# Performance work log

Hardware: AMD Instinct MI355X
Metric: run time of the kernel (lower is better)

## Reference

```python
import jax, jax.numpy as jnp
import numpy as np

B, S, D, H = 16, 577, 768, 12  # batch, seq (24*24+1 cls), hidden, heads
WH, WW = 24, 24
HEAD = D // H
NUM_REL = (2 * WH - 1) * (2 * WW - 1) + 3  # 2212


def make_rel_pos_index(wh, ww):
    # mirrors TFData2VecVisionRelativePositionBias.get_position_index
    xx, yy = np.meshgrid(np.arange(wh), np.arange(ww))  # 'xy' indexing like tf.meshgrid
    coords = np.stack([yy, xx], axis=0).reshape(2, -1)  # [2, wh*ww]
    rel = coords[:, :, None] - coords[:, None, :]       # [2, N, N]
    rel = rel.transpose(1, 2, 0)                        # [N, N, 2]
    rx = (rel[:, :, 0] + wh - 1) * (2 * ww - 1)
    ry = rel[:, :, 1] + ww - 1
    idx = rx + ry                                       # [N, N]
    n = idx.shape[0]
    top = np.full((1, n), NUM_REL - 3, dtype=idx.dtype)
    left = np.full((n, 1), NUM_REL - 2, dtype=idx.dtype)
    corner = np.full((1, 1), NUM_REL - 1, dtype=idx.dtype)
    idx = np.concatenate([top, idx], axis=0)
    idx = np.concatenate([np.concatenate([corner, left], axis=0), idx], axis=1)
    return idx.astype(np.int32)  # [N+1, N+1]


def setup_inputs() -> dict:
    key = jax.random.key(0)
    ks = jax.random.split(key, 6)
    scale = 0.02
    return {
        "hidden_states": jax.random.normal(ks[0], (B, S, D), jnp.float32),
        "Wq": jax.random.normal(ks[1], (D, D), jnp.float32) * scale,
        "bq": jnp.zeros((D,), jnp.float32),
        "Wk": jax.random.normal(ks[2], (D, D), jnp.float32) * scale,
        "Wv": jax.random.normal(ks[3], (D, D), jnp.float32) * scale,
        "bv": jnp.zeros((D,), jnp.float32),
        "rel_pos_bias_table": jax.random.normal(ks[4], (NUM_REL, H), jnp.float32) * scale,
        "rel_pos_index": jnp.asarray(make_rel_pos_index(WH, WW)),
    }


def reference(hidden_states, Wq, bq, Wk, Wv, bv, rel_pos_bias_table, rel_pos_index):
    b, s, _ = hidden_states.shape
    q = (hidden_states @ Wq + bq).reshape(b, s, H, HEAD).transpose(0, 2, 1, 3)
    k = (hidden_states @ Wk).reshape(b, s, H, HEAD).transpose(0, 2, 1, 3)
    v = (hidden_states @ Wv + bv).reshape(b, s, H, HEAD).transpose(0, 2, 1, 3)
    scores = jnp.einsum("bhqd,bhkd->bhqk", q, k) / jnp.sqrt(jnp.float32(HEAD))
    # gathered relative position bias: [S, S, H] -> [H, S, S]
    bias = rel_pos_bias_table[rel_pos_index].transpose(2, 0, 1)
    scores = scores + bias[None]
    probs = jax.nn.softmax(scores, axis=-1)
    out = jnp.einsum("bhqk,bhkd->bhqd", probs, v)
    out = out.transpose(0, 2, 1, 3).reshape(b, s, D)
    return out
```

## Files before the change

kernel.cpp:

```cpp
#include <hip/hip_runtime.h>
#include <hip/hip_bf16.h>


typedef __attribute__((ext_vector_type(8))) short bf16x8;
typedef __attribute__((ext_vector_type(4))) float f32x4;
typedef unsigned short u16;

#define SEQ 577
#define MTOT 9232
#define QKV_STRIDE 7090176
#define VT_PITCH 640
#define B_PITCH 640

static __device__ __forceinline__ u16 f2bf(float x) {
  unsigned int u = __float_as_uint(x);
  u = (u + 0x7FFFu + ((u >> 16) & 1u)) >> 16;
  return (u16)u;
}
static __device__ __forceinline__ float bf2f(u16 v) {
  return __uint_as_float(((unsigned int)v) << 16);
}

static __device__ __forceinline__ void gload_lds16(const void* g, void* l) {
  __builtin_amdgcn_global_load_lds(
      (const __attribute__((address_space(1))) unsigned int*)g,
      (__attribute__((address_space(3))) unsigned int*)l, 16, 0, 0);
}

__global__ __launch_bounds__(256) void transpose_w(
    const float* __restrict__ Wq, const float* __restrict__ Wk,
    const float* __restrict__ Wv, u16* __restrict__ WT) {
  __shared__ float t[32][33];
  const float* W = (blockIdx.z == 0) ? Wq : (blockIdx.z == 1) ? Wk : Wv;
  int x = threadIdx.x & 31;
  int y = threadIdx.x >> 5;
  int k0 = blockIdx.x * 32;
  int n0 = blockIdx.y * 32;
#pragma unroll
  for (int i = 0; i < 4; ++i)
    t[y + i * 8][x] = W[(size_t)(k0 + y + i * 8) * 768 + n0 + x];
  __syncthreads();
  u16* o = WT + (size_t)blockIdx.z * 589824;
#pragma unroll
  for (int i = 0; i < 4; ++i)
    o[(size_t)(n0 + y + i * 8) * 768 + k0 + x] = f2bf(t[x][y + i * 8]);
}

__global__ __launch_bounds__(256) void cvt_x(const float* __restrict__ X,
                                             u16* __restrict__ Xb) {
  size_t i = ((size_t)blockIdx.x * 256 + threadIdx.x) * 8;
  if (i >= (size_t)MTOT * 768) return;
  const float4* xp = (const float4*)(X + i);
  float4 a = xp[0], b = xp[1];
  u16 pk[8] = {f2bf(a.x), f2bf(a.y), f2bf(a.z), f2bf(a.w),
               f2bf(b.x), f2bf(b.y), f2bf(b.z), f2bf(b.w)};
  *(int4*)(Xb + i) = *(const int4*)pk;
}

__global__ __launch_bounds__(256) void bias_pre(
    const float* __restrict__ table, const int* __restrict__ idx,
    u16* __restrict__ biasm) {
  int q = blockIdx.x;
  int h = blockIdx.y;
  for (int k = threadIdx.x; k < B_PITCH; k += 256) {
    u16 v = 0;
    if (k < SEQ) v = f2bf(table[idx[q * SEQ + k] * 12 + h]);
    biasm[((size_t)h * SEQ + q) * B_PITCH + k] = v;
  }
}

__global__ __launch_bounds__(256) void transpose_v(
    const u16* __restrict__ v,
    u16* __restrict__ vT) {
  const int tile = blockIdx.x;
  const int bh = blockIdx.y;
  const int b = bh / 12, h = bh % 12;
  const int tid = threadIdx.x;
  __shared__ u16 T[128][64];
  const int s0 = tile * 128;
  const u16* vp = v + (size_t)b * SEQ * 768 + h * 64;
#pragma unroll
  for (int it = 0; it < 4; ++it) {
    int c = tid + it * 256;
    int r = c >> 3, ko = (c & 7) << 3;
    int gs = s0 + r;
    int4 val = make_int4(0, 0, 0, 0);
    if (gs < SEQ) val = *(const int4*)(vp + (size_t)gs * 768 + ko);
    *(int4*)&T[r][ko ^ (((r >> 3) & 7) << 3)] = val;
  }
  __syncthreads();
  u16* op = vT + (size_t)bh * 64 * VT_PITCH;
#pragma unroll
  for (int it = 0; it < 4; ++it) {
    int c = tid + it * 256;
    int d = c >> 4, so = (c & 15) << 3;
    u16 tmp[8];
#pragma unroll
    for (int j = 0; j < 8; ++j) {
      int rr = so + j;
      tmp[j] = T[rr][d ^ (((rr >> 3) & 7) << 3)];
    }
    *(int4*)(op + (size_t)d * VT_PITCH + s0 + so) = *(const int4*)tmp;
  }
}

__global__ __launch_bounds__(256) void qkv_gemm(
    const u16* __restrict__ Xb,
    const u16* __restrict__ WT,
    const float* __restrict__ bq, const float* __restrict__ bv,
    u16* __restrict__ qkv) {
  const int widx = blockIdx.z;
  const int m0 = blockIdx.x * 128;
  const int n0 = blockIdx.y * 128;
  const int tid = threadIdx.x;
  const int lane = tid & 63;
  const int w = tid >> 6;
  const int wm = (w >> 1) * 64;
  const int wn = (w & 1) * 64;
  const int quad = lane >> 4;
  const int l15 = lane & 15;

  __shared__ u16 As[128][32];
  __shared__ u16 Bs[128][32];

  const u16* Wp = WT + (size_t)widx * 589824;

  const int srow = w * 32 + (lane >> 2);
  const int scol = (lane & 3) * 8;

  f32x4 acc[4][4];
#pragma unroll
  for (int i = 0; i < 4; ++i)
#pragma unroll
    for (int j = 0; j < 4; ++j) acc[i][j] = (f32x4){0.f, 0.f, 0.f, 0.f};

  for (int kt = 0; kt < 24; ++kt) {
    const int k0 = kt * 32;
    {
      int r0 = m0 + srow;
      int r1 = r0 + 16;
      if (r0 > MTOT - 1) r0 = MTOT - 1;
      if (r1 > MTOT - 1) r1 = MTOT - 1;
      gload_lds16(Xb + (size_t)r0 * 768 + k0 + scol, &As[w * 32][0]);
      gload_lds16(Xb + (size_t)r1 * 768 + k0 + scol, &As[w * 32 + 16][0]);
      gload_lds16(Wp + (size_t)(n0 + srow) * 768 + k0 + scol, &Bs[w * 32][0]);
      gload_lds16(Wp + (size_t)(n0 + srow + 16) * 768 + k0 + scol, &Bs[w * 32 + 16][0]);
    }
    __syncthreads();
    bf16x8 af[4], bfv[4];
#pragma unroll
    for (int i = 0; i < 4; ++i)
      af[i] = *(const bf16x8*)(&As[wm + i * 16 + l15][quad * 8]);
#pragma unroll
    for (int i = 0; i < 4; ++i)
      bfv[i] = *(const bf16x8*)(&Bs[wn + i * 16 + l15][quad * 8]);
#pragma unroll
    for (int mt = 0; mt < 4; ++mt)
#pragma unroll
      for (int nt = 0; nt < 4; ++nt)
        acc[mt][nt] = __builtin_amdgcn_mfma_f32_16x16x32_bf16(af[mt], bfv[nt],
                                                              acc[mt][nt], 0, 0, 0);
    __syncthreads();
  }

  const float scale = (widx == 0) ? 0.125f : 1.0f;
  u16* ob = qkv + (size_t)widx * QKV_STRIDE;
#pragma unroll
  for (int nt = 0; nt < 4; ++nt) {
    int n = n0 + wn + nt * 16 + l15;
    float biasv = 0.f;
    if (widx == 0) biasv = bq[n] * 0.125f;
    else if (widx == 2) biasv = bv[n];
#pragma unroll
    for (int mt = 0; mt < 4; ++mt) {
#pragma unroll
      for (int r = 0; r < 4; ++r) {
        int m = m0 + wm + mt * 16 + quad * 4 + r;
        if (m < MTOT)
          ob[(size_t)m * 768 + n] = f2bf(acc[mt][nt][r] * scale + biasv);
      }
    }
  }
}

__global__ __launch_bounds__(256) void attn(
    const u16* __restrict__ qkv, const u16* __restrict__ vT,
    const u16* __restrict__ biasm, float* __restrict__ out) {
  const int bh = blockIdx.x;
  const int qt = blockIdx.y;
  const int b = bh / 12, h = bh - b * 12;
  const int tid = threadIdx.x;
  const int lane = tid & 63;
  const int w = tid >> 6;
  const int quad = lane >> 4;
  const int l15 = lane & 15;

  const u16* qp = qkv + (size_t)b * SEQ * 768 + h * 64;
  const u16* kp = qp + (size_t)QKV_STRIDE;
  const u16* vtp = vT + (size_t)bh * 64 * VT_PITCH;
  const u16* bp = biasm + (size_t)h * SEQ * B_PITCH;

  __shared__ u16 Ks[64][72];
  __shared__ u16 VTs[64][72];
  __shared__ u16 Ps[4][16][72];

  const int qrow0 = qt * 64 + w * 16;

  bf16x8 qf[2];
  {
    int row = qrow0 + l15;
    if (row > 576) row = 576;
    qf[0] = *(const bf16x8*)(qp + (size_t)row * 768 + quad * 8);
    qf[1] = *(const bf16x8*)(qp + (size_t)row * 768 + 32 + quad * 8);
  }
  int brow[4];
#pragma unroll
  for (int r = 0; r < 4; ++r) {
    int rr = qrow0 + quad * 4 + r;
    if (rr > 576) rr = 576;
    brow[r] = rr;
  }

  float lacc[4] = {0.f, 0.f, 0.f, 0.f};
  f32x4 O[4];
#pragma unroll
  for (int dt = 0; dt < 4; ++dt) O[dt] = (f32x4){0.f, 0.f, 0.f, 0.f};

  for (int kt = 0; kt < 10; ++kt) {
    const int kbase = kt * 64;
    u16 bb[4][4];
#pragma unroll
    for (int nt = 0; nt < 4; ++nt)
#pragma unroll
      for (int r = 0; r < 4; ++r)
        bb[nt][r] = bp[(size_t)brow[r] * B_PITCH + kbase + nt * 16 + l15];

#pragma unroll
    for (int it = 0; it < 2; ++it) {
      int c = tid + it * 256;
      int rr = c >> 3, ko = (c & 7) << 3;
      int gk = kbase + rr;
      int4 kvv = make_int4(0, 0, 0, 0);
      if (gk < SEQ) kvv = *(const int4*)(kp + (size_t)gk * 768 + ko);
      *(int4*)&Ks[rr][ko] = kvv;
      *(int4*)&VTs[rr][ko] = *(const int4*)(vtp + (size_t)rr * VT_PITCH + kbase + ko);
    }
    __syncthreads();

    f32x4 s[4];
#pragma unroll
    for (int nt = 0; nt < 4; ++nt) {
      f32x4 z = (f32x4){bf2f(bb[nt][0]), bf2f(bb[nt][1]),
                        bf2f(bb[nt][2]), bf2f(bb[nt][3])};
      bf16x8 kf0 = *(const bf16x8*)(&Ks[nt * 16 + l15][quad * 8]);
      bf16x8 kf1 = *(const bf16x8*)(&Ks[nt * 16 + l15][32 + quad * 8]);
      z = __builtin_amdgcn_mfma_f32_16x16x32_bf16(qf[0], kf0, z, 0, 0, 0);
      z = __builtin_amdgcn_mfma_f32_16x16x32_bf16(qf[1], kf1, z, 0, 0, 0);
      s[nt] = z;
    }

    const bool full = (kbase + 64 <= SEQ);
#pragma unroll
    for (int nt = 0; nt < 4; ++nt) {
#pragma unroll
      for (int r = 0; r < 4; ++r) {
        float p = __expf(s[nt][r]);
        unsigned int u = __float_as_uint(p);
        float pt = __uint_as_float(u & 0xFFFF0000u);
        if (full) lacc[r] += pt;
        else lacc[r] += ((kbase + nt * 16 + l15) < SEQ) ? pt : 0.f;
        Ps[w][quad * 4 + r][((nt ^ quad) << 4) + l15] = (u16)(u >> 16);
      }
    }

#pragma unroll
    for (int ks = 0; ks < 2; ++ks) {
      int cc = (ks * 32 + quad * 8) ^ ((l15 >> 2) << 4);
      bf16x8 pf = *(const bf16x8*)(&Ps[w][l15][cc]);
#pragma unroll
      for (int dt = 0; dt < 4; ++dt) {
        bf16x8 vf = *(const bf16x8*)(&VTs[dt * 16 + l15][ks * 32 + quad * 8]);
        O[dt] = __builtin_amdgcn_mfma_f32_16x16x32_bf16(pf, vf, O[dt], 0, 0, 0);
      }
    }
    __syncthreads();
  }

#pragma unroll
  for (int r = 0; r < 4; ++r) {
    float l = lacc[r];
    l += __shfl_xor(l, 1);
    l += __shfl_xor(l, 2);
    l += __shfl_xor(l, 4);
    l += __shfl_xor(l, 8);
    int row = qrow0 + quad * 4 + r;
    if (row < SEQ) {
      float inv = 1.f / l;
#pragma unroll
      for (int dt = 0; dt < 4; ++dt)
        out[((size_t)(b * SEQ + row)) * 768 + h * 64 + dt * 16 + l15] = O[dt][r] * inv;
    }
  }
}

extern "C" void kernel_launch(void* const* d_in, const int* in_sizes, int n_in,
                              void* d_out, int out_size, void* d_ws, size_t ws_size,
                              hipStream_t stream) {
  const float* hs = (const float*)d_in[0];
  const float* Wq = (const float*)d_in[1];
  const float* bq = (const float*)d_in[2];
  const float* Wk = (const float*)d_in[3];
  const float* Wv = (const float*)d_in[4];
  const float* bv = (const float*)d_in[5];
  const float* table = (const float*)d_in[6];
  const int* idx = (const int*)d_in[7];
  float* out = (float*)d_out;

  char* ws = (char*)d_ws;
  u16* qkv = (u16*)ws;
  u16* WT = (u16*)(ws + 42541056);
  u16* Xb = (u16*)(ws + 46080000);
  u16* vT = (u16*)(ws + 42541056);
  u16* biasm = (u16*)(ws + 58269696);

  hipLaunchKernelGGL(transpose_w, dim3(24, 24, 3), dim3(256), 0, stream, Wq, Wk, Wv, WT);
  hipLaunchKernelGGL(cvt_x, dim3(3462), dim3(256), 0, stream, hs, Xb);
  hipLaunchKernelGGL(qkv_gemm, dim3(73, 6, 3), dim3(256), 0, stream, Xb, WT, bq, bv, qkv);
  hipLaunchKernelGGL(bias_pre, dim3(577, 12), dim3(256), 0, stream, table, idx, biasm);
  hipLaunchKernelGGL(transpose_v, dim3(5, 192), dim3(256), 0, stream,
                     qkv + 2 * (size_t)QKV_STRIDE, vT);
  hipLaunchKernelGGL(attn, dim3(192, 10), dim3(256), 0, stream, qkv, vT, biasm, out);
}
```

Measured before the change: 237.2 us.

## Remap QKV GEMM blocks per XCD and stage epilogue through LDS for vector stores

The QKV GEMM launch becomes a 1D grid whose block index is remapped so that all 18 N/weight tiles of a given M row-tile run on the same XCD. This is meant to improve L2 reuse of the X tile. The epilogue now writes the bf16 results into a swizzled LDS buffer, reused from the operand tiles, in two halves, then emits 16-byte coalesced global stores instead of scattered 2-byte stores. The cost is extra barriers, some idle padded blocks (1440 launched versus 1314 needed), and only half the waves active during each LDS write phase.

```diff
diff --git a/kernel.cpp b/kernel.cpp
--- a/kernel.cpp
+++ b/kernel.cpp
@@ -109,9 +109,16 @@
     const u16* __restrict__ WT,
     const float* __restrict__ bq, const float* __restrict__ bv,
     u16* __restrict__ qkv) {
-  const int widx = blockIdx.z;
-  const int m0 = blockIdx.x * 128;
-  const int n0 = blockIdx.y * 128;
+  const int bid = blockIdx.x;
+  const int xcd = bid & 7;
+  const int local = bid >> 3;
+  const int mp = (local / 18) * 8 + xcd;
+  if (mp >= 73) return;
+  const int nw = local % 18;
+  const int widx = nw % 3;
+  const int m0 = mp * 128;
+  const int n0 = (nw / 3) * 128;
+
   const int tid = threadIdx.x;
   const int lane = tid & 63;
   const int w = tid >> 6;
@@ -120,8 +127,7 @@
   const int quad = lane >> 4;
   const int l15 = lane & 15;
 
-  __shared__ u16 As[128][32];
-  __shared__ u16 Bs[128][32];
+  __shared__ u16 SH[2][128][32];
 
   const u16* Wp = WT + (size_t)widx * 589824;
 
@@ -141,19 +147,19 @@
       int r1 = r0 + 16;
       if (r0 > MTOT - 1) r0 = MTOT - 1;
       if (r1 > MTOT - 1) r1 = MTOT - 1;
-      gload_lds16(Xb + (size_t)r0 * 768 + k0 + scol, &As[w * 32][0]);
-      gload_lds16(Xb + (size_t)r1 * 768 + k0 + scol, &As[w * 32 + 16][0]);
-      gload_lds16(Wp + (size_t)(n0 + srow) * 768 + k0 + scol, &Bs[w * 32][0]);
-      gload_lds16(Wp + (size_t)(n0 + srow + 16) * 768 + k0 + scol, &Bs[w * 32 + 16][0]);
+      gload_lds16(Xb + (size_t)r0 * 768 + k0 + scol, &SH[0][w * 32][0]);
+      gload_lds16(Xb + (size_t)r1 * 768 + k0 + scol, &SH[0][w * 32 + 16][0]);
+      gload_lds16(Wp + (size_t)(n0 + srow) * 768 + k0 + scol, &SH[1][w * 32][0]);
+      gload_lds16(Wp + (size_t)(n0 + srow + 16) * 768 + k0 + scol, &SH[1][w * 32 + 16][0]);
     }
     __syncthreads();
     bf16x8 af[4], bfv[4];
 #pragma unroll
     for (int i = 0; i < 4; ++i)
-      af[i] = *(const bf16x8*)(&As[wm + i * 16 + l15][quad * 8]);
+      af[i] = *(const bf16x8*)(&SH[0][wm + i * 16 + l15][quad * 8]);
 #pragma unroll
     for (int i = 0; i < 4; ++i)
-      bfv[i] = *(const bf16x8*)(&Bs[wn + i * 16 + l15][quad * 8]);
+      bfv[i] = *(const bf16x8*)(&SH[1][wn + i * 16 + l15][quad * 8]);
 #pragma unroll
     for (int mt = 0; mt < 4; ++mt)
 #pragma unroll
@@ -165,21 +171,40 @@
 
   const float scale = (widx == 0) ? 0.125f : 1.0f;
   u16* ob = qkv + (size_t)widx * QKV_STRIDE;
+  float biasv[4];
 #pragma unroll
   for (int nt = 0; nt < 4; ++nt) {
     int n = n0 + wn + nt * 16 + l15;
-    float biasv = 0.f;
-    if (widx == 0) biasv = bq[n] * 0.125f;
-    else if (widx == 2) biasv = bv[n];
-#pragma unroll
-    for (int mt = 0; mt < 4; ++mt) {
-#pragma unroll
-      for (int r = 0; r < 4; ++r) {
-        int m = m0 + wm + mt * 16 + quad * 4 + r;
-        if (m < MTOT)
-          ob[(size_t)m * 768 + n] = f2bf(acc[mt][nt][r] * scale + biasv);
+    biasv[nt] = (widx == 0) ? bq[n] * 0.125f : (widx == 2) ? bv[n] : 0.f;
+  }
+  u16* S = &SH[0][0][0];
+#pragma unroll
+  for (int half = 0; half < 2; ++half) {
+    if ((w >> 1) == half) {
+#pragma unroll
+      for (int mt = 0; mt < 4; ++mt)
+#pragma unroll
+        for (int nt = 0; nt < 4; ++nt)
+#pragma unroll
+          for (int r = 0; r < 4; ++r) {
+            int rowl = mt * 16 + quad * 4 + r;
+            int col = wn + nt * 16 + l15;
+            int cs = (col + quad * 32) & 127;
+            S[rowl * 128 + cs] = f2bf(acc[mt][nt][r] * scale + biasv[nt]);
+          }
+    }
+    __syncthreads();
+#pragma unroll
+    for (int it = 0; it < 4; ++it) {
+      int c = tid + it * 256;
+      int rowl = c >> 4, ch = c & 15;
+      int m = m0 + half * 64 + rowl;
+      if (m < MTOT) {
+        int cs = (ch * 8 + ((rowl >> 2) & 3) * 32) & 127;
+        *(int4*)(ob + (size_t)m * 768 + n0 + ch * 8) = *(const int4*)&S[rowl * 128 + cs];
       }
     }
+    __syncthreads();
   }
 }
 
@@ -325,7 +350,7 @@
 
   hipLaunchKernelGGL(transpose_w, dim3(24, 24, 3), dim3(256), 0, stream, Wq, Wk, Wv, WT);
   hipLaunchKernelGGL(cvt_x, dim3(3462), dim3(256), 0, stream, hs, Xb);
-  hipLaunchKernelGGL(qkv_gemm, dim3(73, 6, 3), dim3(256), 0, stream, Xb, WT, bq, bv, qkv);
+  hipLaunchKernelGGL(qkv_gemm, dim3(1440), dim3(256), 0, stream, Xb, WT, bq, bv, qkv);
   hipLaunchKernelGGL(bias_pre, dim3(577, 12), dim3(256), 0, stream, table, idx, biasm);
   hipLaunchKernelGGL(transpose_v, dim3(5, 192), dim3(256), 0, stream,
                      qkv + 2 * (size_t)QKV_STRIDE, vT);
```

Result: faster. 221.2 us (-6.7%).
